# Performance work log

Hardware: AMD Instinct MI355X
Metric: run time of the kernel (lower is better)

## Reference

```python
import jax, jax.numpy as jnp
import numpy as np

B, N, L = 16, 128, 512            # batch, scan length, per-step feature (= configs.seq_len)
D, S, K, R, H = 1024, 16, 4, 64, 2048  # d_model, d_state, ker_size, dt_rank, hidden_dimention


def _mamba_params(key, scale=0.02):
    ks = jax.random.split(key, 6)
    return dict(
        in_w=jax.random.normal(ks[0], (2 * D, L)) * scale,
        conv_w=jax.random.normal(ks[1], (D, K)) * scale,
        conv_b=jnp.zeros((D,)),
        xproj_w=jax.random.normal(ks[2], (R + 2 * S, D)) * scale,
        dt_w=jax.random.normal(ks[3], (D, R)) * scale,
        dt_b=jax.random.normal(ks[4], (D,)) * scale,
        A_log=jnp.tile(jnp.log(jnp.arange(1, S + 1, dtype=jnp.float32)), (D, 1)),
        Dp=jnp.ones((D,)),
        out_w=jax.random.normal(ks[5], (L, D)) * scale,
    )


def setup_inputs():
    key = jax.random.key(0)
    kx, kf, kr, k1, k2 = jax.random.split(key, 5)
    inp = {"x": jax.random.normal(kx, (B, N, L), dtype=jnp.float32)}
    for pre, k in (("f_", kf), ("r_", kr)):
        for n, v in _mamba_params(k).items():
            inp[pre + n] = v
    inp["pu_w"] = jax.random.normal(k1, (H, L)) * 0.02
    inp["pu_b"] = jnp.zeros((H,))
    inp["pl_w"] = jax.random.normal(k2, (L, H)) * 0.02
    inp["pl_b"] = jnp.zeros((L,))
    inp["ln_g"] = jnp.ones((L,))
    inp["ln_b"] = jnp.zeros((L,))
    return inp


def _ln(x, g, b, eps=1e-5):
    m = x.mean(-1, keepdims=True)
    v = ((x - m) ** 2).mean(-1, keepdims=True)
    return (x - m) * jax.lax.rsqrt(v + eps) * g + b


def _dw_causal_conv(x, w, b):
    # x: [B,N,D]; depthwise causal conv along N with kernel [D,K]
    xt = jnp.pad(x.transpose(0, 2, 1), ((0, 0), (0, 0), (K - 1, 0)))  # [B,D,N+K-1]
    y = jax.lax.conv_general_dilated(xt, w[:, None, :], (1,), 'VALID',
                                     dimension_numbers=('NCH', 'OIH', 'NCH'),
                                     feature_group_count=D)
    return (y + b[None, :, None]).transpose(0, 2, 1)


def _mamba(x, in_w, conv_w, conv_b, xproj_w, dt_w, dt_b, A_log, Dp, out_w):
    # standard Mamba block (in_proj -> depthwise conv -> silu -> selective scan -> gate -> out_proj)
    xi, res = jnp.split(x @ in_w.T, 2, axis=-1)             # [B,N,D] each
    xc = jax.nn.silu(_dw_causal_conv(xi, conv_w, conv_b))   # [B,N,D]
    dbc = xc @ xproj_w.T                                    # [B,N,R+2S]
    dt, Bm, Cm = dbc[..., :R], dbc[..., R:R + S], dbc[..., R + S:]
    delta = jax.nn.softplus(dt @ dt_w.T + dt_b)             # [B,N,D]
    A = -jnp.exp(A_log)                                     # [D,S]
    dA = jnp.exp(delta[..., None] * A)                      # [B,N,D,S]
    dBx = delta[..., None] * Bm[:, :, None, :] * xc[..., None]

    def step(h, t):
        dA_t, dBx_t, C_t = t
        h = dA_t * h + dBx_t                                # [B,D,S]
        return h, jnp.einsum('bds,bs->bd', h, C_t)

    _, ys = jax.lax.scan(step, jnp.zeros((x.shape[0], D, S), x.dtype),
                         (dA.transpose(1, 0, 2, 3), dBx.transpose(1, 0, 2, 3), Cm.transpose(1, 0, 2)))
    y = ys.transpose(1, 0, 2) + xc * Dp                     # [B,N,D]
    y = y * jax.nn.silu(res)
    return y @ out_w.T                                      # [B,N,L]


def reference(x, f_in_w, f_conv_w, f_conv_b, f_xproj_w, f_dt_w, f_dt_b, f_A_log, f_Dp, f_out_w,
              r_in_w, r_conv_w, r_conv_b, r_xproj_w, r_dt_w, r_dt_b, r_A_log, r_Dp, r_out_w,
              pu_w, pu_b, pl_w, pl_b, ln_g, ln_b):
    y1 = _mamba(x, f_in_w, f_conv_w, f_conv_b, f_xproj_w, f_dt_w, f_dt_b, f_A_log, f_Dp, f_out_w)
    y2 = _mamba(x[:, ::-1, :], r_in_w, r_conv_w, r_conv_b, r_xproj_w, r_dt_w, r_dt_b, r_A_log, r_Dp, r_out_w)
    y3 = _ln(x + y1 + y2[:, ::-1, :], ln_g, ln_b)
    yp = jax.nn.relu(y3 @ pu_w.T + pu_b)
    yp = yp @ pl_w.T + pl_b
    return _ln(yp + y3, ln_g, ln_b)
```

## Files before the change

### kernel.cpp

```cpp
#include <hip/hip_runtime.h>
#include <hip/hip_bf16.h>
#include <cstdint>

typedef __hip_bfloat16 bf16;

constexpr int Bb = 16, Nn = 128, Ll = 512, Dd = 1024, Ss = 16, Rr = 64, Hh = 2048;
constexpr int Mm = Bb * Nn;
#define LOG2E 1.44269504088896340736f

using bf16x8 = __attribute__((ext_vector_type(8))) __bf16;
using bf16x4 = __attribute__((ext_vector_type(4))) __bf16;
using f32x4  = __attribute__((ext_vector_type(4))) float;

__device__ __forceinline__ float to_f(float x) { return x; }
__device__ __forceinline__ float to_f(bf16 x) { return __bfloat162float(x); }
__device__ __forceinline__ void store_t(float* p, float v) { *p = v; }
__device__ __forceinline__ void store_t(bf16* p, float v) { *p = __float2bfloat16(v); }
__device__ __forceinline__ __bf16 cvt1(float x) {
  bf16 h = __float2bfloat16(x);
  return *reinterpret_cast<__bf16*>(&h);
}
__device__ __forceinline__ float bfraw_to_f(__bf16 x) {
  bf16 h = *reinterpret_cast<bf16*>(&x);
  return __bfloat162float(h);
}
__device__ __forceinline__ bf16x8 load8(const bf16* p) { return *(const bf16x8*)p; }
__device__ __forceinline__ bf16x8 load8(const float* p) {
  float4 a = *(const float4*)p;
  float4 b = *(const float4*)(p + 4);
  bf16x8 r;
  r[0] = cvt1(a.x); r[1] = cvt1(a.y); r[2] = cvt1(a.z); r[3] = cvt1(a.w);
  r[4] = cvt1(b.x); r[5] = cvt1(b.y); r[6] = cvt1(b.z); r[7] = cvt1(b.w);
  return r;
}
__device__ __forceinline__ bf16x8 load8rt(const void* p, size_t idx, int isbf) {
  if (isbf) return load8((const bf16*)p + idx);
  return load8((const float*)p + idx);
}
__device__ __forceinline__ float ldf(const void* p, int i, int isbf) {
  if (isbf) return __bfloat162float(((const bf16*)p)[i]);
  return ((const float*)p)[i];
}

enum { EPI_STORE = 0, EPI_BIAS_RELU = 1, EPI_ADD = 3, EPI_BIAS = 4, EPI_BIAS_SOFTPLUS = 5,
       EPI_ATOMIC = 6 };

__global__ void sniff_kernel(const unsigned short* __restrict__ xs, int* __restrict__ flags) {
  const int tid = threadIdx.x;
  int cnt = 0;
  for (int j = 0; j < 64; ++j) {
    int i = tid + j * 256;
    unsigned short u = xs[(size_t)i * 64];
    bf16 h = *reinterpret_cast<bf16*>(&u);
    float v = __bfloat162float(h);
    float a = fabsf(v);
    if (v == 0.f || (a > 0.0009765625f && a < 16.f)) ++cnt;
  }
  __shared__ int sc[256];
  sc[tid] = cnt;
  __syncthreads();
  for (int o = 128; o > 0; o >>= 1) {
    if (tid < o) sc[tid] += sc[tid + o];
    __syncthreads();
  }
  if (tid == 0) flags[0] = (sc[0] > 8192) ? 1 : 0;
}

constexpr int LDT2 = 72;

template <typename TC, int EPI>
__global__ __launch_bounds__(256) void gemm_rt(
    const int* __restrict__ flagp,
    const void* __restrict__ A, int lda, int abf,
    const void* __restrict__ Bw, const void* __restrict__ Bw2, int ldb,
    int bmode, int bsplit,
    TC* __restrict__ C, int ldc,
    const void* __restrict__ bias, const void* __restrict__ bias2,
    int N, int Kchunk, int zk, size_t a_doff, size_t c_doff) {
  const int isbf = *flagp;
  const int ab = (abf == 2) ? isbf : abf;
  __shared__ __align__(16) __bf16 As[64 * LDT2];
  __shared__ __align__(16) __bf16 Bs[64 * LDT2];
  const int tid = threadIdx.x;
  const int wave = tid >> 6, lane = tid & 63;
  const int quad = lane >> 4, l16 = lane & 15;
  const int wm = wave & 1, wn = wave >> 1;
  int bx = blockIdx.x, by = blockIdx.y;
  const int gx = gridDim.x, gy = gridDim.y;
  if ((gx & 7) == 0) {
    int id = bx + gx * by;
    int xcd = id & 7, sl = id >> 3;
    by = sl % gy;
    bx = (sl / gy) * 8 + xcd;
  }
  int zsl = blockIdx.z;
  const void* Ap = A;
  const void* Bp0 = Bw;
  const void* biasp = bias;
  if (bmode == 3) {
    const int dir = zsl / zk;
    zsl = zsl % zk;
    if (dir) {
      Ap = (const char*)A + a_doff * (size_t)(ab ? 2 : 4);
      C += c_doff;
      Bp0 = Bw2;
      biasp = bias2;
    }
  }
  const int m0 = by * 64, n0 = bx * 64;
  const int kb = zsl * Kchunk;
  const int srow = tid >> 3;
  const int scol = (tid & 7) * 8;
  f32x4 acc[2][2] = {};
  for (int k0 = kb; k0 < kb + Kchunk; k0 += 64) {
#pragma unroll
    for (int h = 0; h < 2; ++h) {
      int r = srow + h * 32;
      *(bf16x8*)(&As[r * LDT2 + scol]) =
          load8rt(Ap, (size_t)(m0 + r) * lda + k0 + scol, ab);
      int rb = n0 + r;
      rb = rb < N ? rb : N - 1;
      const void* bp = Bp0;
      size_t bi;
      const int kk = k0 + scol;
      if (bmode == 1 && rb >= bsplit) {
        bp = Bw2; bi = (size_t)(rb - bsplit) * ldb + kk;
      } else if (bmode == 2 && kk >= bsplit) {
        bp = Bw2; bi = (size_t)rb * ldb + (kk - bsplit);
      } else {
        bi = (size_t)rb * ldb + kk;
      }
      *(bf16x8*)(&Bs[r * LDT2 + scol]) = load8rt(bp, bi, isbf);
    }
    __syncthreads();
#pragma unroll
    for (int kk2 = 0; kk2 < 2; ++kk2) {
      bf16x8 af[2], bfr[2];
#pragma unroll
      for (int i = 0; i < 2; ++i)
        af[i] = *(const bf16x8*)(&As[(wm * 32 + i * 16 + l16) * LDT2 + kk2 * 32 + quad * 8]);
#pragma unroll
      for (int j = 0; j < 2; ++j)
        bfr[j] = *(const bf16x8*)(&Bs[(wn * 32 + j * 16 + l16) * LDT2 + kk2 * 32 + quad * 8]);
#pragma unroll
      for (int i = 0; i < 2; ++i)
#pragma unroll
        for (int j = 0; j < 2; ++j)
          acc[i][j] = __builtin_amdgcn_mfma_f32_16x16x32_bf16(af[i], bfr[j], acc[i][j], 0, 0, 0);
    }
    __syncthreads();
  }
#pragma unroll
  for (int i = 0; i < 2; ++i) {
#pragma unroll
    for (int j = 0; j < 2; ++j) {
      const int col = n0 + wn * 32 + j * 16 + l16;
      if (col >= N) continue;
      float bv = 0.f;
      if (EPI == EPI_BIAS_RELU || EPI == EPI_BIAS || EPI == EPI_BIAS_SOFTPLUS)
        bv = ldf(biasp, col, isbf);
#pragma unroll
      for (int r = 0; r < 4; ++r) {
        const int row = m0 + wm * 32 + i * 16 + quad * 4 + r;
        size_t idx = (size_t)row * ldc + col;
        float v = acc[i][j][r];
        if (EPI == EPI_STORE) store_t(&C[idx], v);
        else if (EPI == EPI_BIAS_RELU) { v += bv; store_t(&C[idx], v > 0.f ? v : 0.f); }
        else if (EPI == EPI_BIAS) store_t(&C[idx], v + bv);
        else if (EPI == EPI_BIAS_SOFTPLUS) {
          v += bv;
          store_t(&C[idx], (v > 20.f) ? v : log1pf(__expf(v)));
        } else if (EPI == EPI_ATOMIC) {
          atomicAdd((float*)&C[idx], v);
        }
      }
    }
  }
}

__global__ __launch_bounds__(256) void init_merge_rt(const int* __restrict__ flagp,
                                                     const void* __restrict__ x,
                                                     float* __restrict__ ZB,
                                                     float* __restrict__ zerop,
                                                     int nzb4, int nzero4) {
  const int isbf = *flagp;
  int i = blockIdx.x * 256 + threadIdx.x;
  if (i < nzb4) {
    float4 o;
    if (isbf) {
      ushort4 u = ((const ushort4*)x)[i];
      bf16 h0 = *reinterpret_cast<bf16*>(&u.x), h1 = *reinterpret_cast<bf16*>(&u.y);
      bf16 h2 = *reinterpret_cast<bf16*>(&u.z), h3 = *reinterpret_cast<bf16*>(&u.w);
      o = float4{__bfloat162float(h0), __bfloat162float(h1),
                 __bfloat162float(h2), __bfloat162float(h3)};
    } else {
      o = ((const float4*)x)[i];
    }
    ((float4*)ZB)[i] = o;
  } else {
    int j = i - nzb4;
    if (j < nzero4) ((float4*)zerop)[j] = float4{0.f, 0.f, 0.f, 0.f};
  }
}

__global__ __launch_bounds__(256) void conv_silu_rt(
    const int* __restrict__ flagp, const bf16* __restrict__ X2b,
    const void* __restrict__ fcw, const void* __restrict__ fcb,
    const void* __restrict__ rcw, const void* __restrict__ rcb,
    bf16* __restrict__ XCb) {
  const int isbf = *flagp;
  const int dir = blockIdx.y >> 2;
  const int d = (blockIdx.y & 3) * 256 + threadIdx.x;
  const int m = blockIdx.x;
  const int t = m & (Nn - 1);
  const void* cw = dir ? rcw : fcw;
  const void* cb = dir ? rcb : fcb;
  float w0 = ldf(cw, d * 4 + 0, isbf), w1 = ldf(cw, d * 4 + 1, isbf);
  float w2 = ldf(cw, d * 4 + 2, isbf), w3 = ldf(cw, d * 4 + 3, isbf);
  float a = ldf(cb, d, isbf);
  const size_t base = (size_t)m * 4096 + (size_t)dir * 2048 + d;
  if (dir == 0) {
    if (t >= 3) a += w0 * to_f(X2b[base - 3 * 4096]);
    if (t >= 2) a += w1 * to_f(X2b[base - 2 * 4096]);
    if (t >= 1) a += w2 * to_f(X2b[base - 1 * 4096]);
    a += w3 * to_f(X2b[base]);
  } else {
    if (t + 3 < Nn) a += w0 * to_f(X2b[base + 3 * 4096]);
    if (t + 2 < Nn) a += w1 * to_f(X2b[base + 2 * 4096]);
    if (t + 1 < Nn) a += w2 * to_f(X2b[base + 1 * 4096]);
    a += w3 * to_f(X2b[base]);
  }
  const float s = a / (1.f + __builtin_amdgcn_exp2f(-a * LOG2E));
  XCb[(size_t)m * 2048 + (size_t)dir * 1024 + d] = __float2bfloat16(s);
}

__global__ __launch_bounds__(128) void scan_gate3(
    const int* __restrict__ flagp,
    const float* __restrict__ DBC0, bf16* __restrict__ XCb, const bf16* __restrict__ X2b,
    const bf16* __restrict__ DELTA0,
    const void* __restrict__ fAlog, const void* __restrict__ fDp,
    const void* __restrict__ rAlog, const void* __restrict__ rDp) {
  const int isbf = *flagp;
  const int dir = blockIdx.z;
  const float* DBC = DBC0 + (size_t)dir * Mm * 96;
  const bf16* DELTA = DELTA0 + (size_t)dir * Mm * 1024;
  const void* A_log = dir ? rAlog : fAlog;
  const void* Dp = dir ? rDp : fDp;
  __shared__ __align__(16) __bf16 sBC[Nn * 32];
  __shared__ __align__(16) __bf16 sD[Nn * 32];
  __shared__ __align__(16) __bf16 sX[Nn * 32];
  __shared__ __align__(16) __bf16 sG[Nn * 32];
  const int b = blockIdx.x;
  const int d0 = blockIdx.y * 32;
  const int tid = threadIdx.x;
  const size_t rowbase = (size_t)b * Nn;
  const size_t xc_col = (size_t)dir * 1024;
#pragma unroll
  for (int k = 0; k < 8; ++k) {
    int idx = tid + k * 128;
    int t = idx >> 3, c = idx & 7;
    float4 v = *(const float4*)(DBC + (rowbase + t) * 96 + 64 + c * 4);
    bf16x4 pv = {cvt1(v.x), cvt1(v.y), cvt1(v.z), cvt1(v.w)};
    int dst = (c < 4) ? (t * 32 + c * 8) : (t * 32 + (c - 4) * 8 + 4);
    *(bf16x4*)&sBC[dst] = pv;
  }
#pragma unroll
  for (int k = 0; k < 4; ++k) {
    int idx = tid + k * 128;
    int t = idx >> 2, h = idx & 3;
    *(uint4*)&sD[t * 32 + h * 8] =
        *(const uint4*)(DELTA + (rowbase + t) * 1024 + d0 + h * 8);
    *(uint4*)&sX[t * 32 + h * 8] =
        *(const uint4*)(XCb + (rowbase + t) * 2048 + xc_col + d0 + h * 8);
    bf16x8 rv = *(const bf16x8*)(X2b + (rowbase + t) * 4096 + (size_t)dir * 2048 + 1024 + d0 + h * 8);
    bf16x8 gv;
#pragma unroll
    for (int e = 0; e < 8; ++e) {
      float r = bfraw_to_f(rv[e]);
      gv[e] = cvt1(r / (1.f + __builtin_amdgcn_exp2f(-r * LOG2E)));
    }
    *(bf16x8*)&sG[t * 32 + h * 8] = gv;
  }
  __syncthreads();
  const int wv = tid >> 6, lane = tid & 63;
  const int dl = lane & 15, sg = lane >> 4;
  const int d_local = wv * 16 + dl;
  const int d = d0 + d_local;
  float A_[4];
#pragma unroll
  for (int j = 0; j < 4; ++j)
    A_[j] = -__expf(ldf(A_log, d * Ss + sg * 4 + j, isbf)) * LOG2E;
  const float dp = ldf(Dp, d, isbf);
  float h0 = 0.f, h1 = 0.f, h2 = 0.f, h3 = 0.f;
  for (int p = 0; p < Nn; ++p) {
    const int t = dir ? (Nn - 1 - p) : p;
    const float dv = bfraw_to_f(sD[t * 32 + d_local]);
    const float xv = bfraw_to_f(sX[t * 32 + d_local]);
    bf16x8 bc = *(const bf16x8*)&sBC[t * 32 + sg * 8];
    const float dx = dv * xv;
    h0 = __builtin_amdgcn_exp2f(dv * A_[0]) * h0 + dx * bfraw_to_f(bc[0]);
    h1 = __builtin_amdgcn_exp2f(dv * A_[1]) * h1 + dx * bfraw_to_f(bc[1]);
    h2 = __builtin_amdgcn_exp2f(dv * A_[2]) * h2 + dx * bfraw_to_f(bc[2]);
    h3 = __builtin_amdgcn_exp2f(dv * A_[3]) * h3 + dx * bfraw_to_f(bc[3]);
    float acc = h0 * bfraw_to_f(bc[4]) + h1 * bfraw_to_f(bc[5]) +
                h2 * bfraw_to_f(bc[6]) + h3 * bfraw_to_f(bc[7]);
    acc += __shfl_xor(acc, 16, 64);
    acc += __shfl_xor(acc, 32, 64);
    if (sg == 0) {
      const float g = bfraw_to_f(sG[t * 32 + d_local]);
      XCb[(rowbase + t) * 2048 + xc_col + d] = __float2bfloat16((acc + xv * dp) * g);
    }
  }
}

template <int MODE>
__global__ __launch_bounds__(256) void ln_rt(const int* __restrict__ flagp,
                                             const float* __restrict__ Z,
                                             const float* __restrict__ Zadd,
                                             const void* __restrict__ g,
                                             const void* __restrict__ bb,
                                             const void* __restrict__ pb,
                                             void* __restrict__ outp,
                                             bf16* __restrict__ outp2) {
  const int isbf = *flagp;
  const int row = blockIdx.x;
  const int tid = threadIdx.x;
  const int c0 = tid * 2;
  const float2* z = (const float2*)(Z + (size_t)row * Ll);
  float2 v = z[tid];
  if (MODE == 1) {
    const float2* za = (const float2*)(Zadd + (size_t)row * Ll);
    float2 a = za[tid];
    v.x += a.x + ldf(pb, c0, isbf);
    v.y += a.y + ldf(pb, c0 + 1, isbf);
  }
  float s = v.x + v.y, q = v.x * v.x + v.y * v.y;
#pragma unroll
  for (int o = 32; o > 0; o >>= 1) {
    s += __shfl_xor(s, o, 64);
    q += __shfl_xor(q, o, 64);
  }
  __shared__ float ss[4], qq[4];
  const int wv = tid >> 6, ln = tid & 63;
  if (ln == 0) { ss[wv] = s; qq[wv] = q; }
  __syncthreads();
  s = ss[0] + ss[1] + ss[2] + ss[3];
  q = qq[0] + qq[1] + qq[2] + qq[3];
  const float mean = s * (1.f / Ll);
  const float var = q * (1.f / Ll) - mean * mean;
  const float rs = rsqrtf(var + 1e-5f);
  const float o0 = (v.x - mean) * rs * ldf(g, c0, isbf) + ldf(bb, c0, isbf);
  const float o1 = (v.y - mean) * rs * ldf(g, c0 + 1, isbf) + ldf(bb, c0 + 1, isbf);
  if (MODE == 0) {
    float* out = (float*)outp;
    out[(size_t)row * Ll + c0] = o0;
    out[(size_t)row * Ll + c0 + 1] = o1;
    outp2[(size_t)row * Ll + c0] = __float2bfloat16(o0);
    outp2[(size_t)row * Ll + c0 + 1] = __float2bfloat16(o1);
  } else {
    if (isbf) {
      bf16* out = (bf16*)outp;
      out[(size_t)row * Ll + c0] = __float2bfloat16(o0);
      out[(size_t)row * Ll + c0 + 1] = __float2bfloat16(o1);
    } else {
      float* out = (float*)outp;
      out[(size_t)row * Ll + c0] = o0;
      out[(size_t)row * Ll + c0 + 1] = o1;
    }
  }
}

extern "C" void kernel_launch(void* const* d_in, const int* in_sizes, int n_in, void* d_out,
                              int out_size, void* d_ws, size_t ws_size, hipStream_t stream) {
  char* ws = (char*)d_ws;
  int* flags = (int*)ws;
  bf16* X2b = (bf16*)(ws + 256);
  bf16* XCb = X2b + (size_t)Mm * 4096;
  float* DBC = (float*)(XCb + (size_t)Mm * 2048);
  float* Z2 = DBC + (size_t)2 * Mm * 96;
  float* ZB = Z2 + (size_t)Mm * 512;
  float* Y3 = ZB + (size_t)Mm * 512;
  bf16* Y3b = (bf16*)(Y3 + (size_t)Mm * 512);
  bf16* DELTA = Y3b + (size_t)Mm * 512;
  bf16* H1 = X2b;
  size_t needed = 256 +
                  2 * ((size_t)Mm * 4096 + (size_t)Mm * 2048 + (size_t)Mm * 512 +
                       (size_t)2 * Mm * 1024) +
                  4 * ((size_t)2 * Mm * 96 + (size_t)3 * Mm * 512);
  if (ws_size < needed) return;

  const void* x = d_in[0];
  const dim3 blk(256);
  const int nzb4 = Mm * Ll / 4;
  const int nzero4 = (2 * Mm * 96 + Mm * 512) / 4;

  sniff_kernel<<<dim3(1), blk, 0, stream>>>((const unsigned short*)x, flags);
  init_merge_rt<<<dim3((nzb4 + nzero4 + 255) / 256), blk, 0, stream>>>(
      flags, x, ZB, DBC, nzb4, nzero4);
  gemm_rt<bf16, EPI_STORE><<<dim3(64, 32), blk, 0, stream>>>(
      flags, x, Ll, 2, d_in[1], d_in[10], Ll, 1, 2048,
      X2b, 4096, nullptr, nullptr, 4096, Ll, 1, 0, 0);
  conv_silu_rt<<<dim3(Mm, 8), blk, 0, stream>>>(flags, X2b, d_in[2], d_in[3],
                                                d_in[11], d_in[12], XCb);
  gemm_rt<float, EPI_ATOMIC><<<dim3(2, 32, 8), blk, 0, stream>>>(
      flags, XCb, 2048, 1, d_in[4], d_in[13], Dd, 3, 0,
      DBC, 96, nullptr, nullptr, 96, 256, 4, 1024, (size_t)Mm * 96);
  gemm_rt<bf16, EPI_BIAS_SOFTPLUS><<<dim3(16, 32, 2), blk, 0, stream>>>(
      flags, DBC, 96, 0, d_in[5], d_in[14], Rr, 3, 0,
      DELTA, 1024, d_in[6], d_in[15], 1024, Rr, 1, (size_t)Mm * 96, (size_t)Mm * 1024);
  scan_gate3<<<dim3(Bb, Dd / 32, 2), dim3(128), 0, stream>>>(
      flags, DBC, XCb, X2b, DELTA, d_in[7], d_in[8], d_in[16], d_in[17]);
  gemm_rt<float, EPI_ATOMIC><<<dim3(8, 32, 4), blk, 0, stream>>>(
      flags, XCb, 2048, 1, d_in[9], d_in[18], Dd, 2, 1024,
      ZB, Ll, nullptr, nullptr, Ll, 512, 1, 0, 0);
  ln_rt<0><<<dim3(Mm), blk, 0, stream>>>(flags, ZB, nullptr, d_in[23], d_in[24], nullptr,
                                         (void*)Y3, Y3b);
  gemm_rt<bf16, EPI_BIAS_RELU><<<dim3(32, 32), blk, 0, stream>>>(
      flags, Y3b, Ll, 1, d_in[19], nullptr, Ll, 0, 0,
      H1, Hh, d_in[20], nullptr, Hh, Ll, 1, 0, 0);
  gemm_rt<float, EPI_ATOMIC><<<dim3(8, 32, 2), blk, 0, stream>>>(
      flags, H1, Hh, 1, d_in[21], nullptr, Hh, 0, 0,
      Z2, Ll, nullptr, nullptr, Ll, 1024, 1, 0, 0);
  ln_rt<1><<<dim3(Mm), blk, 0, stream>>>(flags, Z2, Y3, d_in[23], d_in[24], d_in[22],
                                         d_out, nullptr);

  (void)in_sizes; (void)n_in; (void)out_size;
}
```

Baseline: 352.2 us.

## Add 128x128 direct-to-LDS GEMM, pre-convert weights to bf16, unroll scan by four

Adds a new 128x128-tile GEMM that loads bf16 operands straight into LDS with global_load_lds and remaps blocks across XCDs. It is used for in_proj, out_proj and both MLP GEMMs. A new kernel converts the weights to bf16 on every call, with the out_proj weights concatenated, and the input is emitted as bf16 so the GEMMs skip per-load conversion and branching. The scan loop is grouped four steps at a time so the cross-lane reductions and stores are batched. The cost is an extra weight-conversion pass each call, more workspace, and the removal of B-split handling from gemm_rt.

Measured after the change: 322.7 us. 8.4% less time.

```diff
diff --git a/kernel.cpp b/kernel.cpp
--- a/kernel.cpp
+++ b/kernel.cpp
@@ -40,6 +40,11 @@
 __device__ __forceinline__ float ldf(const void* p, int i, int isbf) {
   if (isbf) return __bfloat162float(((const bf16*)p)[i]);
   return ((const float*)p)[i];
+}
+__device__ __forceinline__ void gld16(const bf16* g, __bf16* l) {
+  __builtin_amdgcn_global_load_lds(
+      (const __attribute__((address_space(1))) void*)g,
+      (__attribute__((address_space(3))) void*)l, 16, 0, 0);
 }
 
 enum { EPI_STORE = 0, EPI_BIAS_RELU = 1, EPI_ADD = 3, EPI_BIAS = 4, EPI_BIAS_SOFTPLUS = 5,
@@ -64,6 +69,34 @@
     __syncthreads();
   }
   if (tid == 0) flags[0] = (sc[0] > 8192) ? 1 : 0;
+}
+
+__global__ __launch_bounds__(256) void wconv_kernel(
+    const int* __restrict__ flagp,
+    const void* __restrict__ fin, const void* __restrict__ rin,
+    const void* __restrict__ fout, const void* __restrict__ rout,
+    const void* __restrict__ puw, const void* __restrict__ plw,
+    bf16* __restrict__ WBin, bf16* __restrict__ WBout,
+    bf16* __restrict__ WBpu, bf16* __restrict__ WBpl) {
+  const int isbf = *flagp;
+  const int i = blockIdx.x * 256 + threadIdx.x;
+  const void* src;
+  bf16* dst;
+  int si;
+  if (i < 131072) { src = fin; si = i; dst = WBin + (size_t)si * 8; }
+  else if (i < 262144) { src = rin; si = i - 131072; dst = WBin + (size_t)1048576 + (size_t)si * 8; }
+  else if (i < 393216) { src = puw; si = i - 262144; dst = WBpu + (size_t)si * 8; }
+  else if (i < 524288) { src = plw; si = i - 393216; dst = WBpl + (size_t)si * 8; }
+  else if (i < 589824) {
+    src = fout; si = i - 524288;
+    int e = si * 8;
+    dst = WBout + (size_t)(e >> 10) * 2048 + (e & 1023);
+  } else {
+    src = rout; si = i - 589824;
+    int e = si * 8;
+    dst = WBout + (size_t)(e >> 10) * 2048 + 1024 + (e & 1023);
+  }
+  *(bf16x8*)dst = load8rt(src, (size_t)si * 8, isbf);
 }
 
 constexpr int LDT2 = 72;
@@ -120,17 +153,8 @@
           load8rt(Ap, (size_t)(m0 + r) * lda + k0 + scol, ab);
       int rb = n0 + r;
       rb = rb < N ? rb : N - 1;
-      const void* bp = Bp0;
-      size_t bi;
-      const int kk = k0 + scol;
-      if (bmode == 1 && rb >= bsplit) {
-        bp = Bw2; bi = (size_t)(rb - bsplit) * ldb + kk;
-      } else if (bmode == 2 && kk >= bsplit) {
-        bp = Bw2; bi = (size_t)rb * ldb + (kk - bsplit);
-      } else {
-        bi = (size_t)rb * ldb + kk;
-      }
-      *(bf16x8*)(&Bs[r * LDT2 + scol]) = load8rt(bp, bi, isbf);
+      size_t bi = (size_t)rb * ldb + k0 + scol;
+      *(bf16x8*)(&Bs[r * LDT2 + scol]) = load8rt(Bp0, bi, isbf);
     }
     __syncthreads();
 #pragma unroll
@@ -178,25 +202,105 @@
   }
 }
 
+template <typename TC, int EPI>
+__global__ __launch_bounds__(256) void gemm128n(
+    const int* __restrict__ flagp,
+    const bf16* __restrict__ A, int lda,
+    const bf16* __restrict__ Bw, int ldb,
+    TC* __restrict__ C, int ldc,
+    const void* __restrict__ bias,
+    int Kchunk) {
+  __shared__ __align__(16) __bf16 As[128 * 64];
+  __shared__ __align__(16) __bf16 Bs[128 * 64];
+  const int tid = threadIdx.x;
+  const int wave = tid >> 6, lane = tid & 63;
+  const int quad = lane >> 4, l16 = lane & 15;
+  const int wr = wave >> 1, wc = wave & 1;
+  int bx = blockIdx.x, by = blockIdx.y;
+  const int gx = gridDim.x, gy = gridDim.y;
+  if ((gx & 7) == 0) {
+    int id = bx + gx * by;
+    int xcd = id & 7, sl = id >> 3;
+    by = sl % gy;
+    bx = (sl / gy) * 8 + xcd;
+  }
+  const int m0 = by * 128, n0 = bx * 128;
+  const int kb = blockIdx.z * Kchunk;
+  const int lr = lane >> 3;
+  const int lc = (lane & 7) * 8;
+  f32x4 acc[4][4] = {};
+  for (int k0 = kb; k0 < kb + Kchunk; k0 += 64) {
+#pragma unroll
+    for (int rr = 0; rr < 4; ++rr) {
+      const int rowb = rr * 32 + wave * 8;
+      gld16(A + (size_t)(m0 + rowb + lr) * lda + k0 + lc, &As[rowb * 64]);
+      gld16(Bw + (size_t)(n0 + rowb + lr) * ldb + k0 + lc, &Bs[rowb * 64]);
+    }
+    __syncthreads();
+#pragma unroll
+    for (int kk = 0; kk < 2; ++kk) {
+      bf16x8 af[4], bfr[4];
+#pragma unroll
+      for (int i = 0; i < 4; ++i)
+        af[i] = *(const bf16x8*)(&As[(wr * 64 + i * 16 + l16) * 64 + kk * 32 + quad * 8]);
+#pragma unroll
+      for (int j = 0; j < 4; ++j)
+        bfr[j] = *(const bf16x8*)(&Bs[(wc * 64 + j * 16 + l16) * 64 + kk * 32 + quad * 8]);
+#pragma unroll
+      for (int i = 0; i < 4; ++i)
+#pragma unroll
+        for (int j = 0; j < 4; ++j)
+          acc[i][j] = __builtin_amdgcn_mfma_f32_16x16x32_bf16(af[i], bfr[j], acc[i][j], 0, 0, 0);
+    }
+    __syncthreads();
+  }
+  const int isbf = *flagp;
+#pragma unroll
+  for (int i = 0; i < 4; ++i) {
+#pragma unroll
+    for (int j = 0; j < 4; ++j) {
+      const int col = n0 + wc * 64 + j * 16 + l16;
+      float bv = 0.f;
+      if (EPI == EPI_BIAS_RELU) bv = ldf(bias, col, isbf);
+#pragma unroll
+      for (int r = 0; r < 4; ++r) {
+        const int row = m0 + wr * 64 + i * 16 + quad * 4 + r;
+        size_t idx = (size_t)row * ldc + col;
+        float v = acc[i][j][r];
+        if (EPI == EPI_STORE) store_t(&C[idx], v);
+        else if (EPI == EPI_BIAS_RELU) { v += bv; store_t(&C[idx], v > 0.f ? v : 0.f); }
+        else if (EPI == EPI_ATOMIC) atomicAdd((float*)&C[idx], v);
+      }
+    }
+  }
+}
+
 __global__ __launch_bounds__(256) void init_merge_rt(const int* __restrict__ flagp,
                                                      const void* __restrict__ x,
                                                      float* __restrict__ ZB,
+                                                     unsigned short* __restrict__ Xb,
                                                      float* __restrict__ zerop,
                                                      int nzb4, int nzero4) {
   const int isbf = *flagp;
   int i = blockIdx.x * 256 + threadIdx.x;
   if (i < nzb4) {
     float4 o;
+    ushort4 u;
     if (isbf) {
-      ushort4 u = ((const ushort4*)x)[i];
+      u = ((const ushort4*)x)[i];
       bf16 h0 = *reinterpret_cast<bf16*>(&u.x), h1 = *reinterpret_cast<bf16*>(&u.y);
       bf16 h2 = *reinterpret_cast<bf16*>(&u.z), h3 = *reinterpret_cast<bf16*>(&u.w);
       o = float4{__bfloat162float(h0), __bfloat162float(h1),
                  __bfloat162float(h2), __bfloat162float(h3)};
     } else {
       o = ((const float4*)x)[i];
+      bf16 h0 = __float2bfloat16(o.x), h1 = __float2bfloat16(o.y);
+      bf16 h2 = __float2bfloat16(o.z), h3 = __float2bfloat16(o.w);
+      u = ushort4{*(unsigned short*)&h0, *(unsigned short*)&h1,
+                  *(unsigned short*)&h2, *(unsigned short*)&h3};
     }
     ((float4*)ZB)[i] = o;
+    ((ushort4*)Xb)[i] = u;
   } else {
     int j = i - nzb4;
     if (j < nzero4) ((float4*)zerop)[j] = float4{0.f, 0.f, 0.f, 0.f};
@@ -292,23 +396,35 @@
     A_[j] = -__expf(ldf(A_log, d * Ss + sg * 4 + j, isbf)) * LOG2E;
   const float dp = ldf(Dp, d, isbf);
   float h0 = 0.f, h1 = 0.f, h2 = 0.f, h3 = 0.f;
-  for (int p = 0; p < Nn; ++p) {
-    const int t = dir ? (Nn - 1 - p) : p;
-    const float dv = bfraw_to_f(sD[t * 32 + d_local]);
-    const float xv = bfraw_to_f(sX[t * 32 + d_local]);
-    bf16x8 bc = *(const bf16x8*)&sBC[t * 32 + sg * 8];
-    const float dx = dv * xv;
-    h0 = __builtin_amdgcn_exp2f(dv * A_[0]) * h0 + dx * bfraw_to_f(bc[0]);
-    h1 = __builtin_amdgcn_exp2f(dv * A_[1]) * h1 + dx * bfraw_to_f(bc[1]);
-    h2 = __builtin_amdgcn_exp2f(dv * A_[2]) * h2 + dx * bfraw_to_f(bc[2]);
-    h3 = __builtin_amdgcn_exp2f(dv * A_[3]) * h3 + dx * bfraw_to_f(bc[3]);
-    float acc = h0 * bfraw_to_f(bc[4]) + h1 * bfraw_to_f(bc[5]) +
+  for (int pg = 0; pg < Nn / 4; ++pg) {
+    float accs[4], xvs[4];
+#pragma unroll
+    for (int u = 0; u < 4; ++u) {
+      const int p = pg * 4 + u;
+      const int t = dir ? (Nn - 1 - p) : p;
+      const float dv = bfraw_to_f(sD[t * 32 + d_local]);
+      const float xv = bfraw_to_f(sX[t * 32 + d_local]);
+      bf16x8 bc = *(const bf16x8*)&sBC[t * 32 + sg * 8];
+      const float dx = dv * xv;
+      h0 = __builtin_amdgcn_exp2f(dv * A_[0]) * h0 + dx * bfraw_to_f(bc[0]);
+      h1 = __builtin_amdgcn_exp2f(dv * A_[1]) * h1 + dx * bfraw_to_f(bc[1]);
+      h2 = __builtin_amdgcn_exp2f(dv * A_[2]) * h2 + dx * bfraw_to_f(bc[2]);
+      h3 = __builtin_amdgcn_exp2f(dv * A_[3]) * h3 + dx * bfraw_to_f(bc[3]);
+      accs[u] = h0 * bfraw_to_f(bc[4]) + h1 * bfraw_to_f(bc[5]) +
                 h2 * bfraw_to_f(bc[6]) + h3 * bfraw_to_f(bc[7]);
-    acc += __shfl_xor(acc, 16, 64);
-    acc += __shfl_xor(acc, 32, 64);
-    if (sg == 0) {
-      const float g = bfraw_to_f(sG[t * 32 + d_local]);
-      XCb[(rowbase + t) * 2048 + xc_col + d] = __float2bfloat16((acc + xv * dp) * g);
+      xvs[u] = xv;
+    }
+#pragma unroll
+    for (int u = 0; u < 4; ++u) {
+      float a = accs[u];
+      a += __shfl_xor(a, 16, 64);
+      a += __shfl_xor(a, 32, 64);
+      if (sg == 0) {
+        const int p = pg * 4 + u;
+        const int t = dir ? (Nn - 1 - p) : p;
+        const float g = bfraw_to_f(sG[t * 32 + d_local]);
+        XCb[(rowbase + t) * 2048 + xc_col + d] = __float2bfloat16((a + xvs[u] * dp) * g);
+      }
     }
   }
 }
@@ -376,16 +492,23 @@
   int* flags = (int*)ws;
   bf16* X2b = (bf16*)(ws + 256);
   bf16* XCb = X2b + (size_t)Mm * 4096;
-  float* DBC = (float*)(XCb + (size_t)Mm * 2048);
+  bf16* Y3b = XCb + (size_t)Mm * 2048;
+  bf16* DELTA = Y3b + (size_t)Mm * 512;
+  bf16* Xb = DELTA + (size_t)2 * Mm * 1024;
+  bf16* WBin = Xb + (size_t)Mm * 512;
+  bf16* WBout = WBin + (size_t)4096 * 512;
+  bf16* WBpu = WBout + (size_t)512 * 2048;
+  bf16* WBpl = WBpu + (size_t)2048 * 512;
+  float* DBC = (float*)(WBpl + (size_t)512 * 2048);
   float* Z2 = DBC + (size_t)2 * Mm * 96;
   float* ZB = Z2 + (size_t)Mm * 512;
   float* Y3 = ZB + (size_t)Mm * 512;
-  bf16* Y3b = (bf16*)(Y3 + (size_t)Mm * 512);
-  bf16* DELTA = Y3b + (size_t)Mm * 512;
   bf16* H1 = X2b;
   size_t needed = 256 +
                   2 * ((size_t)Mm * 4096 + (size_t)Mm * 2048 + (size_t)Mm * 512 +
-                       (size_t)2 * Mm * 1024) +
+                       (size_t)2 * Mm * 1024 + (size_t)Mm * 512 +
+                       (size_t)4096 * 512 + (size_t)512 * 2048 +
+                       (size_t)2048 * 512 + (size_t)512 * 2048) +
                   4 * ((size_t)2 * Mm * 96 + (size_t)3 * Mm * 512);
   if (ws_size < needed) return;
 
@@ -396,10 +519,12 @@
 
   sniff_kernel<<<dim3(1), blk, 0, stream>>>((const unsigned short*)x, flags);
   init_merge_rt<<<dim3((nzb4 + nzero4 + 255) / 256), blk, 0, stream>>>(
-      flags, x, ZB, DBC, nzb4, nzero4);
-  gemm_rt<bf16, EPI_STORE><<<dim3(64, 32), blk, 0, stream>>>(
-      flags, x, Ll, 2, d_in[1], d_in[10], Ll, 1, 2048,
-      X2b, 4096, nullptr, nullptr, 4096, Ll, 1, 0, 0);
+      flags, x, ZB, (unsigned short*)Xb, DBC, nzb4, nzero4);
+  wconv_kernel<<<dim3(2560), blk, 0, stream>>>(
+      flags, d_in[1], d_in[10], d_in[9], d_in[18], d_in[19], d_in[21],
+      WBin, WBout, WBpu, WBpl);
+  gemm128n<bf16, EPI_STORE><<<dim3(32, 16), blk, 0, stream>>>(
+      flags, Xb, Ll, WBin, Ll, X2b, 4096, nullptr, Ll);
   conv_silu_rt<<<dim3(Mm, 8), blk, 0, stream>>>(flags, X2b, d_in[2], d_in[3],
                                                 d_in[11], d_in[12], XCb);
   gemm_rt<float, EPI_ATOMIC><<<dim3(2, 32, 8), blk, 0, stream>>>(
@@ -410,17 +535,14 @@
       DELTA, 1024, d_in[6], d_in[15], 1024, Rr, 1, (size_t)Mm * 96, (size_t)Mm * 1024);
   scan_gate3<<<dim3(Bb, Dd / 32, 2), dim3(128), 0, stream>>>(
       flags, DBC, XCb, X2b, DELTA, d_in[7], d_in[8], d_in[16], d_in[17]);
-  gemm_rt<float, EPI_ATOMIC><<<dim3(8, 32, 4), blk, 0, stream>>>(
-      flags, XCb, 2048, 1, d_in[9], d_in[18], Dd, 2, 1024,
-      ZB, Ll, nullptr, nullptr, Ll, 512, 1, 0, 0);
+  gemm128n<float, EPI_ATOMIC><<<dim3(4, 16, 4), blk, 0, stream>>>(
+      flags, XCb, 2048, WBout, 2048, ZB, Ll, nullptr, Ll);
   ln_rt<0><<<dim3(Mm), blk, 0, stream>>>(flags, ZB, nullptr, d_in[23], d_in[24], nullptr,
                                          (void*)Y3, Y3b);
-  gemm_rt<bf16, EPI_BIAS_RELU><<<dim3(32, 32), blk, 0, stream>>>(
-      flags, Y3b, Ll, 1, d_in[19], nullptr, Ll, 0, 0,
-      H1, Hh, d_in[20], nullptr, Hh, Ll, 1, 0, 0);
-  gemm_rt<float, EPI_ATOMIC><<<dim3(8, 32, 2), blk, 0, stream>>>(
-      flags, H1, Hh, 1, d_in[21], nullptr, Hh, 0, 0,
-      Z2, Ll, nullptr, nullptr, Ll, 1024, 1, 0, 0);
+  gemm128n<bf16, EPI_BIAS_RELU><<<dim3(16, 16), blk, 0, stream>>>(
+      flags, Y3b, Ll, WBpu, Ll, H1, Hh, d_in[20], Ll);
+  gemm128n<float, EPI_ATOMIC><<<dim3(4, 16, 4), blk, 0, stream>>>(
+      flags, H1, Hh, WBpl, 2048, Z2, Ll, nullptr, Ll);
   ln_rt<1><<<dim3(Mm), blk, 0, stream>>>(flags, Z2, Y3, d_in[23], d_in[24], d_in[22],
                                          d_out, nullptr);
 
```
